# Kernel optimization log

Hardware: AMD Instinct MI355X
Metric: run time of the kernel (lower is better)

The kernel has to match this reference:

```python
import jax, jax.numpy as jnp
import numpy as np

B, N, D = 8, 2048, 512


def setup_inputs() -> dict:
    key = jax.random.key(0)
    ks = jax.random.split(key, 16)
    s = 1.0 / np.sqrt(D)  # ~ torch Linear default init scale
    inp = {
        "X": jax.random.normal(ks[0], (B, N, D), jnp.float32),
        "Y": jax.random.normal(ks[1], (B, N, D), jnp.float32),
    }
    names = ["xq", "xk", "xv", "yq", "yk", "yv"]
    for i, nm in enumerate(names):
        inp[f"W_{nm}"] = jax.random.uniform(ks[2 + 2 * i], (D, D), jnp.float32, -s, s)
        inp[f"b_{nm}"] = jax.random.uniform(ks[3 + 2 * i], (D,), jnp.float32, -s, s)
    return inp


def _lin(x, W, b):
    # torch nn.Linear: x @ W^T + b
    return jnp.einsum("bnd,ed->bne", x, W) + b


def reference(X, Y, W_xq, b_xq, W_xk, b_xk, W_xv, b_xv, W_yq, b_yq, W_yk, b_yk, W_yv, b_yv):
    d = X.shape[-1]
    scale = 1.0 / jnp.sqrt(jnp.asarray(d, X.dtype))
    Q1, K1, V1 = _lin(X, W_xq, b_xq), _lin(X, W_xk, b_xk), _lin(X, W_xv, b_xv)
    Q2, K2, V2 = _lin(Y, W_yq, b_yq), _lin(Y, W_yk, b_yk), _lin(Y, W_yv, b_yv)
    # NOTE: F.softmax called without dim on a 3-D tensor -> torch legacy dim=0 (batch axis).
    S1 = jnp.einsum("bnd,bmd->bnm", Q1, K2) * scale  # [B, N, N]
    A1 = jax.nn.softmax(S1, axis=0)
    U_A1 = X + jnp.einsum("bnm,bmd->bnd", A1, V2)  # dropout = identity (eval)
    S2 = jnp.einsum("bnd,bmd->bnm", Q2, K1) * scale
    A2 = jax.nn.softmax(S2, axis=0)
    U_A2 = Y + jnp.einsum("bnm,bmd->bnd", A2, V1)
    return U_A1 + U_A2
```

## Files before the change

### kernel.cpp

```cpp
#include <hip/hip_runtime.h>

typedef unsigned short u16;
typedef unsigned char u8;
typedef __attribute__((ext_vector_type(8))) short bf16x8;
typedef __attribute__((ext_vector_type(4))) float f32x4;
typedef __attribute__((ext_vector_type(8))) u16 u16x8;
typedef __attribute__((ext_vector_type(2))) int i32x2;
typedef __attribute__((ext_vector_type(2))) float f32x2;

#define GLOAD_LDS(g, s) __builtin_amdgcn_global_load_lds( \
    (const __attribute__((address_space(1))) void*)(g),   \
    (__attribute__((address_space(3))) void*)(s), 16, 0, 0)

__device__ __forceinline__ u16 f2bf(float f) {
  union { float f; unsigned u; } v; v.f = f;
  unsigned r = v.u + 0x7fffu + ((v.u >> 16) & 1u);
  return (u16)(r >> 16);
}
__device__ __forceinline__ float bf2f(u16 h) {
  union { unsigned u; float f; } v; v.u = ((unsigned)h) << 16;
  return v.f;
}

__device__ __forceinline__ unsigned lds_addr(const void* p) {
  return (unsigned)(unsigned long long)(__attribute__((address_space(3))) const void*)p;
}
__device__ __forceinline__ bf16x8 ds128(const void* p) {
  bf16x8 r;
  asm volatile("ds_read_b128 %0, %1" : "=v"(r) : "v"(lds_addr(p)));
  return r;
}
__device__ __forceinline__ i32x2 ds64(const void* p) {
  i32x2 r;
  asm volatile("ds_read_b64 %0, %1" : "=v"(r) : "v"(lds_addr(p)));
  return r;
}
__device__ __forceinline__ bf16x8 cvt8(i32x2 v) {
  f32x2 f0 = __builtin_amdgcn_cvt_pk_f32_fp8(v[0], false);
  f32x2 f1 = __builtin_amdgcn_cvt_pk_f32_fp8(v[0], true);
  f32x2 f2 = __builtin_amdgcn_cvt_pk_f32_fp8(v[1], false);
  f32x2 f3 = __builtin_amdgcn_cvt_pk_f32_fp8(v[1], true);
  unsigned w0, w1, w2, w3;
  asm("v_cvt_pk_bf16_f32 %0, %1, %2" : "=v"(w0) : "v"(f0[0]), "v"(f0[1]));
  asm("v_cvt_pk_bf16_f32 %0, %1, %2" : "=v"(w1) : "v"(f1[0]), "v"(f1[1]));
  asm("v_cvt_pk_bf16_f32 %0, %1, %2" : "=v"(w2) : "v"(f2[0]), "v"(f2[1]));
  asm("v_cvt_pk_bf16_f32 %0, %1, %2" : "=v"(w3) : "v"(f3[0]), "v"(f3[1]));
  union { unsigned w[4]; bf16x8 v8; } u;
  u.w[0] = w0; u.w[1] = w1; u.w[2] = w2; u.w[3] = w3;
  return u.v8;
}

__device__ __forceinline__ void stage_one(const u16* g, int ld, u16* d, int tid) {
  int rw = tid >> 3;
  int gs = ((tid & 7) ^ (rw & 7)) << 3;
  int wb = (tid >> 6) << 9;
#pragma unroll
  for (int p = 0; p < 4; p++)
    GLOAD_LDS(g + (long)(p * 64 + rw) * ld + gs, d + p * 4096 + wb);
}

__device__ __forceinline__ void gemm256d(f32x4 (&acc)[8][4],
    const u16* Ag, int lda, const u16* Bg, int ldb, int nk,
    u16* As, u16* Bs, int tid) {
  const int lane = tid & 63, wid = tid >> 6;
  const int wr = (wid >> 2) << 7;
  const int wc = (wid & 3) << 6;
  const int rl = lane & 15, kg = lane >> 4;
  const int swz0 = (kg ^ (rl & 7)) << 3;
  const int rbA = (wr + rl) * 64, rbB = (wc + rl) * 64;

  stage_one(Ag, lda, As, tid);
  stage_one(Bg, ldb, Bs, tid);
  if (nk > 1) stage_one(Ag + 64, lda, As + 16384, tid);

  int ba = 0;
  for (int t = 0; t < nk; ++t) {
    if (t + 1 < nk) asm volatile("s_waitcnt vmcnt(4)" ::: "memory");
    else            asm volatile("s_waitcnt vmcnt(0)" ::: "memory");
    __builtin_amdgcn_s_barrier();
    if (t + 1 < nk)
      stage_one(Bg + (t + 1) * 64, ldb, Bs + ((t + 1) & 1) * 16384, tid);
    if (t + 2 < nk) {
      int nb = ba + 2; if (nb >= 3) nb -= 3;
      stage_one(Ag + (long)(t + 2) * 64, lda, As + nb * 16384, tid);
    }
    const u16* ab = As + ba * 16384 + rbA;
    const u16* bb = Bs + (t & 1) * 16384 + rbB;
#pragma unroll
    for (int kk = 0; kk < 2; kk++) {
      const int sw = swz0 ^ (kk << 5);
      bf16x8 a[8], b[4];
#pragma unroll
      for (int i = 0; i < 8; i++) a[i] = ds128(ab + i * 1024 + sw);
#pragma unroll
      for (int j = 0; j < 4; j++) b[j] = ds128(bb + j * 1024 + sw);
      asm volatile("s_waitcnt lgkmcnt(0)" ::: "memory");
      __builtin_amdgcn_sched_barrier(0);
      __builtin_amdgcn_s_setprio(1);
#pragma unroll
      for (int i = 0; i < 8; i++)
#pragma unroll
        for (int j = 0; j < 4; j++)
          acc[i][j] = __builtin_amdgcn_mfma_f32_16x16x32_bf16(a[i], b[j], acc[i][j], 0, 0, 0);
      __builtin_amdgcn_s_setprio(0);
      __builtin_amdgcn_sched_barrier(0);
    }
    ba = ba + 1; if (ba == 3) ba = 0;
  }
}

__device__ __forceinline__ void stage_A64(const u8* gA, u8* Ad, int tid) {
#pragma unroll
  for (int pass = 0; pass < 2; pass++) {
    int gid = pass * 512 + tid;
    int row = gid >> 2, g = gid & 3;
    GLOAD_LDS(gA + (long)row * 2048 + ((g ^ (row & 3)) << 4), Ad + (gid << 4));
  }
}
__device__ __forceinline__ void stage_B64(const u16* gB, u8* Bd, int tid) {
#pragma unroll
  for (int pass = 0; pass < 2; pass++) {
    int gid = pass * 512 + tid;
    int row = gid >> 3, g = gid & 7;
    GLOAD_LDS(gB + (long)row * 2048 + ((g ^ (row & 7)) << 3), Bd + (gid << 4));
  }
}

__device__ __forceinline__ void gemm_pv8(f32x4 (&acc)[4][4],
    const u8* Ag, const u16* Bg, u8* As, u8* Bs, int tid) {
  const int lane = tid & 63, wid = tid >> 6;
  const int mq = wid >> 1, nh = wid & 1;
  const int rl = lane & 15, kg = lane >> 4;
  const int nk = 16;
  const int abase = (mq * 64 + rl) * 64 + ((kg & 1) << 3);
  const int bbase = (nh * 64 + rl) * 128;

  stage_A64(Ag, As, tid);
  stage_B64(Bg, Bs, tid);
  stage_A64(Ag + 64, As + 16384, tid);
  int ba = 0;
  for (int t = 0; t < nk; ++t) {
    if (t + 1 < nk) asm volatile("s_waitcnt vmcnt(2)" ::: "memory");
    else            asm volatile("s_waitcnt vmcnt(0)" ::: "memory");
    __builtin_amdgcn_s_barrier();
    if (t + 1 < nk) stage_B64(Bg + (t + 1) * 64, Bs + ((t + 1) & 1) * 16384, tid);
    if (t + 2 < nk) {
      int nb = ba + 2; if (nb >= 3) nb -= 3;
      stage_A64(Ag + (long)(t + 2) * 64, As + nb * 16384, tid);
    }
    const u8* ab = As + ba * 16384 + abase;
    const u8* bb = Bs + (t & 1) * 16384 + bbase;
#pragma unroll
    for (int kk = 0; kk < 2; kk++) {
      const int sa = (((kk << 1) + (kg >> 1)) ^ (rl & 3)) << 4;
      const int sb = (((kk << 2) + kg) ^ (rl & 7)) << 4;
      i32x2 ar[4]; bf16x8 bfr[4];
#pragma unroll
      for (int i = 0; i < 4; i++) ar[i] = ds64(ab + i * 1024 + sa);
#pragma unroll
      for (int j = 0; j < 4; j++) bfr[j] = ds128(bb + j * 2048 + sb);
      asm volatile("s_waitcnt lgkmcnt(0)" ::: "memory");
      __builtin_amdgcn_sched_barrier(0);
      bf16x8 a[4];
#pragma unroll
      for (int i = 0; i < 4; i++) a[i] = cvt8(ar[i]);
      __builtin_amdgcn_s_setprio(1);
#pragma unroll
      for (int i = 0; i < 4; i++)
#pragma unroll
        for (int j = 0; j < 4; j++)
          acc[i][j] = __builtin_amdgcn_mfma_f32_16x16x32_bf16(a[i], bfr[j], acc[i][j], 0, 0, 0);
      __builtin_amdgcn_s_setprio(0);
      __builtin_amdgcn_sched_barrier(0);
    }
    ba = ba + 1; if (ba == 3) ba = 0;
  }
}

__global__ __launch_bounds__(256) void k_cvt2(const float* __restrict__ inX,
                                              const float* __restrict__ inY,
                                              u16* __restrict__ oX, u16* __restrict__ oY,
                                              int n8) {
  int i = blockIdx.x * 256 + threadIdx.x;
  const float* in = (i < n8) ? inX : inY;
  u16* out = (i < n8) ? oX : oY;
  int k = (i < n8) ? i : i - n8;
  const float4* pf = (const float4*)in + (long)k * 2;
  float4 a = pf[0], b = pf[1];
  u16x8 o;
  o[0] = f2bf(a.x); o[1] = f2bf(a.y); o[2] = f2bf(a.z); o[3] = f2bf(a.w);
  o[4] = f2bf(b.x); o[5] = f2bf(b.y); o[6] = f2bf(b.z); o[7] = f2bf(b.w);
  *((u16x8*)out + k) = o;
}

struct P6 { const float* p[6]; };
struct O6 { u16* p[6]; };

__global__ __launch_bounds__(256) void k_cvt_w(P6 w, u16* __restrict__ out) {
  int z = blockIdx.y;
  int i = blockIdx.x * 256 + threadIdx.x;
  const float4* pf = (const float4*)w.p[z] + (long)i * 2;
  float4 a = pf[0], b = pf[1];
  u16x8 o;
  o[0] = f2bf(a.x); o[1] = f2bf(a.y); o[2] = f2bf(a.z); o[3] = f2bf(a.w);
  o[4] = f2bf(b.x); o[5] = f2bf(b.y); o[6] = f2bf(b.z); o[7] = f2bf(b.w);
  *((u16x8*)(out + (long)z * 262144) + i) = o;
}

__global__ __launch_bounds__(512) void k_proj2(const u16* __restrict__ Xb, const u16* __restrict__ Yb,
                                               const u16* __restrict__ Wb, P6 bias, O6 dst) {
  __shared__ u16 As[49152], Bs[32768];
  int x = blockIdx.x;
  int swz = (x & 7) * 96 + (x >> 3);
  int grp = swz >= 384;
  int r = grp ? swz - 384 : swz;
  int bm = r / 6, bn = r - bm * 6;
  int tid = threadIdx.x;
  const u16* Ag = (grp ? Yb : Xb) + (long)bm * 256 * 512;
  const u16* Bg = Wb + (long)grp * 786432 + (long)bn * 256 * 512;
  f32x4 acc[8][4] = {};
  gemm256d(acc, Ag, 512, Bg, 512, 8, As, Bs, tid);
  int z = grp * 3 + (bn >> 1);
  const float* bi = bias.p[z];
  u16* D = dst.p[z];
  int lane = tid & 63, wid = tid >> 6;
  int row0 = bm * 256 + ((wid >> 2) << 7) + ((lane >> 4) << 2);
  int colz = (bn & 1) * 256 + ((wid & 3) << 6) + (lane & 15);
  float bj[4];
#pragma unroll
  for (int j = 0; j < 4; j++) bj[j] = bi[colz + (j << 4)];
#pragma unroll
  for (int i = 0; i < 8; i++)
#pragma unroll
    for (int j = 0; j < 4; j++)
#pragma unroll
      for (int rr = 0; rr < 4; rr++)
        D[(long)(row0 + (i << 4) + rr) * 512 + colz + (j << 4)] = f2bf(acc[i][j][rr] + bj[j]);
}

__global__ __launch_bounds__(512) void k_s(const u16* __restrict__ Q, const u16* __restrict__ K,
                                           u16* __restrict__ S) {
  __shared__ u16 As[49152], Bs[32768];
  int x = blockIdx.x;
  int swz = (x & 7) * 64 + (x >> 3);
  int bn = swz & 7, bm = (swz >> 3) & 7, b = swz >> 6;
  int tid = threadIdx.x;
  const u16* Ag = Q + (long)b * 1048576 + (long)bm * 256 * 512;
  const u16* Bg = K + (long)b * 1048576 + (long)bn * 256 * 512;
  f32x4 acc[8][4] = {};
  gemm256d(acc, Ag, 512, Bg, 512, 8, As, Bs, tid);
  u16* D = S + (long)b * 4194304;
  const float scale = 0.04419417382415922f;
  int lane = tid & 63, wid = tid >> 6;
  int row0 = bm * 256 + ((wid >> 2) << 7) + ((lane >> 4) << 2);
  int col0 = bn * 256 + ((wid & 3) << 6) + (lane & 15);
#pragma unroll
  for (int i = 0; i < 8; i++)
#pragma unroll
    for (int j = 0; j < 4; j++)
#pragma unroll
      for (int rr = 0; rr < 4; rr++)
        D[(long)(row0 + (i << 4) + rr) * 2048 + col0 + (j << 4)] = f2bf(acc[i][j][rr] * scale);
}

__global__ __launch_bounds__(256) void k_softmax8(const u16* __restrict__ S,
                                                  u8* __restrict__ A8) {
  int idx = blockIdx.x * 256 + threadIdx.x;
  u16x8 v[8];
#pragma unroll
  for (int b = 0; b < 8; b++) v[b] = *((const u16x8*)(S + (long)b * 4194304) + idx);
  unsigned w0[8], w1[8];
#pragma unroll
  for (int jp = 0; jp < 4; jp++) {
    float va[8], vb[8];
    {
      float e[8], m = -1e30f;
#pragma unroll
      for (int b = 0; b < 8; b++) { e[b] = bf2f(v[b][2 * jp]); m = fmaxf(m, e[b]); }
      float s = 0.f;
#pragma unroll
      for (int b = 0; b < 8; b++) { e[b] = __expf(e[b] - m); s += e[b]; }
      float inv = 1.0f / s;
#pragma unroll
      for (int b = 0; b < 8; b++) va[b] = e[b] * inv;
    }
    {
      float e[8], m = -1e30f;
#pragma unroll
      for (int b = 0; b < 8; b++) { e[b] = bf2f(v[b][2 * jp + 1]); m = fmaxf(m, e[b]); }
      float s = 0.f;
#pragma unroll
      for (int b = 0; b < 8; b++) { e[b] = __expf(e[b] - m); s += e[b]; }
      float inv = 1.0f / s;
#pragma unroll
      for (int b = 0; b < 8; b++) vb[b] = e[b] * inv;
    }
#pragma unroll
    for (int b = 0; b < 8; b++) {
      if (jp == 0)      w0[b] = __builtin_amdgcn_cvt_pk_fp8_f32(va[b], vb[b], 0,     false);
      else if (jp == 1) w0[b] = __builtin_amdgcn_cvt_pk_fp8_f32(va[b], vb[b], w0[b], true);
      else if (jp == 2) w1[b] = __builtin_amdgcn_cvt_pk_fp8_f32(va[b], vb[b], 0,     false);
      else              w1[b] = __builtin_amdgcn_cvt_pk_fp8_f32(va[b], vb[b], w1[b], true);
    }
  }
#pragma unroll
  for (int b = 0; b < 8; b++) {
    i32x2 w; w[0] = (int)w0[b]; w[1] = (int)w1[b];
    *(i32x2*)(A8 + (long)b * 4194304 + (long)idx * 8) = w;
  }
}

__global__ __launch_bounds__(256) void k_tr(const u16* __restrict__ V1, const u16* __restrict__ V2,
                                            u16* __restrict__ T1, u16* __restrict__ T2) {
  __shared__ u16 tile[64][65];
  int z = blockIdx.z;
  const u16* src = (z < 8 ? V1 : V2) + (long)(z & 7) * 1048576;
  u16*       dst = (z < 8 ? T1 : T2) + (long)(z & 7) * 1048576;
  int n0 = blockIdx.x * 64, d0 = blockIdx.y * 64;
  int t = threadIdx.x;
  int r = t >> 2, cs = (t & 3) * 16;
  const u16x8* sp = (const u16x8*)(src + (long)(n0 + r) * 512 + d0 + cs);
  u16x8 a = sp[0], b = sp[1];
#pragma unroll
  for (int jj = 0; jj < 8; jj++) { tile[r][cs + jj] = a[jj]; tile[r][cs + 8 + jj] = b[jj]; }
  __syncthreads();
  u16x8 o0, o1;
#pragma unroll
  for (int jj = 0; jj < 8; jj++) { o0[jj] = tile[cs + jj][r]; o1[jj] = tile[cs + 8 + jj][r]; }
  u16x8* op = (u16x8*)(dst + (long)(d0 + r) * 2048 + n0 + cs);
  op[0] = o0; op[1] = o1;
}

__global__ __launch_bounds__(512) void k_pv8m(const u8* __restrict__ A2, const u16* __restrict__ Vt1,
                                              const u8* __restrict__ A1, const u16* __restrict__ Vt2,
                                              const float* __restrict__ X, const float* __restrict__ Y,
                                              float* __restrict__ out, float* __restrict__ P) {
  __shared__ u8 As[49152], Bs[32768];
  int x = blockIdx.x;
  int swz = (x & 7) * 64 + (x >> 3);
  int b = swz >> 6;
  int r = swz & 63;
  int bn = r & 3, kc = (r >> 2) & 1, bm = r >> 3;
  int tid = threadIdx.x;
  long aoff = (long)b * 4194304 + (long)bm * 256 * 2048 + kc * 1024;
  long voff = (long)b * 1048576 + (long)bn * 128 * 2048 + kc * 1024;
  f32x4 acc[4][4] = {};
  gemm_pv8(acc, A2 + aoff, Vt1 + voff, As, Bs, tid);
  __builtin_amdgcn_s_barrier();
  gemm_pv8(acc, A1 + aoff, Vt2 + voff, As, Bs, tid);
  int lane = tid & 63, wid = tid >> 6;
  int mq = wid >> 1, nh = wid & 1;
  int row0 = bm * 256 + mq * 64 + ((lane >> 4) << 2);
  int col0 = bn * 128 + nh * 64 + (lane & 15);
  long base = (long)b * 1048576;
#pragma unroll
  for (int i = 0; i < 4; i++)
#pragma unroll
    for (int j = 0; j < 4; j++)
#pragma unroll
      for (int rr = 0; rr < 4; rr++) {
        long idx = base + (long)(row0 + (i << 4) + rr) * 512 + col0 + (j << 4);
        float v = acc[i][j][rr];
        if (kc) P[idx] = v;
        else    out[idx] = v + X[idx] + Y[idx];
      }
}

__global__ __launch_bounds__(256) void k_fin(float* __restrict__ out, const float* __restrict__ P) {
  long i = (long)(blockIdx.x * 256 + threadIdx.x) * 4;
  float4 o = *(const float4*)(out + i);
  float4 p = *(const float4*)(P + i);
  o.x += p.x; o.y += p.y; o.z += p.z; o.w += p.w;
  *(float4*)(out + i) = o;
}

extern "C" void kernel_launch(void* const* d_in, const int* in_sizes, int n_in,
                              void* d_out, int out_size, void* d_ws, size_t ws_size,
                              hipStream_t stream) {
  const float* X = (const float*)d_in[0];
  const float* Y = (const float*)d_in[1];
  P6 wp, bp;
  for (int i = 0; i < 6; i++) { wp.p[i] = (const float*)d_in[2 + 2 * i]; bp.p[i] = (const float*)d_in[3 + 2 * i]; }

  const long NX = 8L * 2048 * 512;
  const long NS = 8L * 2048 * 2048;
  u16* p = (u16*)d_ws;
  u16* Xb = p;  p += NX;
  u16* Yb = p;  p += NX;
  u16* Wb = p;  p += 6L * 512 * 512;
  u16* Q1 = p;  p += NX;
  u16* K2 = p;  p += NX;
  u16* Q2 = p;  p += NX;
  u16* K1 = p;  p += NX;
  u16* Sb = p;  p += NS;
  u16* V1 = Sb;
  u16* V2 = Sb + NX;
  u16* Vt1 = Xb;
  u16* Vt2 = Yb;
  u8* A8_2 = (u8*)Q2;
  u8* A8_1 = (u8*)Q1;
  float* Pbuf = (float*)Sb;
  (void)ws_size; (void)in_sizes; (void)n_in; (void)out_size;

  dim3 T(256);
  k_cvt2<<<dim3(8192), T, 0, stream>>>(X, Y, Xb, Yb, (int)(NX / 8));
  k_cvt_w<<<dim3(128, 6), T, 0, stream>>>(wp, Wb);
  O6 dst; dst.p[0] = Q1; dst.p[1] = K1; dst.p[2] = V1; dst.p[3] = Q2; dst.p[4] = K2; dst.p[5] = V2;
  k_proj2<<<dim3(768), dim3(512), 0, stream>>>(Xb, Yb, Wb, bp, dst);
  k_tr<<<dim3(32, 8, 16), T, 0, stream>>>(V1, V2, Vt1, Vt2);
  k_s<<<dim3(512), dim3(512), 0, stream>>>(Q2, K1, Sb);
  k_softmax8<<<dim3(2048), T, 0, stream>>>(Sb, A8_2);
  k_s<<<dim3(512), dim3(512), 0, stream>>>(Q1, K2, Sb);
  k_softmax8<<<dim3(2048), T, 0, stream>>>(Sb, A8_1);
  k_pv8m<<<dim3(512), dim3(512), 0, stream>>>(A8_2, Vt1, A8_1, Vt2, X, Y, (float*)d_out, Pbuf);
  k_fin<<<dim3((int)(NX / 1024)), T, 0, stream>>>((float*)d_out, Pbuf);
}
```

Baseline: 335.6 us.

## Permute FP8 attention layout so PV GEMM reads A with one 128-bit LDS load

The softmax kernel now writes FP8 attention weights in a permuted column order, so each lane's two k-halves sit next to each other. The PV GEMM can then fetch A with a single ds_read_b128 per row instead of two ds_read_b64, using an adjusted XOR swizzle on both staging and reading. The k-loop is restructured to issue all LDS reads up front and wait only partially (lgkmcnt(4)) before the first MFMA half, overlapping the second B reads with compute. This couples the producer layout to the consumer, and holding more fragments live raises register pressure.

```diff
diff --git a/kernel.cpp b/kernel.cpp
--- a/kernel.cpp
+++ b/kernel.cpp
@@ -6,6 +6,7 @@
 typedef __attribute__((ext_vector_type(4))) float f32x4;
 typedef __attribute__((ext_vector_type(8))) u16 u16x8;
 typedef __attribute__((ext_vector_type(2))) int i32x2;
+typedef __attribute__((ext_vector_type(4))) int i32x4;
 typedef __attribute__((ext_vector_type(2))) float f32x2;
 
 #define GLOAD_LDS(g, s) __builtin_amdgcn_global_load_lds( \
@@ -30,9 +31,9 @@
   asm volatile("ds_read_b128 %0, %1" : "=v"(r) : "v"(lds_addr(p)));
   return r;
 }
-__device__ __forceinline__ i32x2 ds64(const void* p) {
-  i32x2 r;
-  asm volatile("ds_read_b64 %0, %1" : "=v"(r) : "v"(lds_addr(p)));
+__device__ __forceinline__ i32x4 ds128i(const void* p) {
+  i32x4 r;
+  asm volatile("ds_read_b128 %0, %1" : "=v"(r) : "v"(lds_addr(p)));
   return r;
 }
 __device__ __forceinline__ bf16x8 cvt8(i32x2 v) {
@@ -114,7 +115,7 @@
   for (int pass = 0; pass < 2; pass++) {
     int gid = pass * 512 + tid;
     int row = gid >> 2, g = gid & 3;
-    GLOAD_LDS(gA + (long)row * 2048 + ((g ^ (row & 3)) << 4), Ad + (gid << 4));
+    GLOAD_LDS(gA + (long)row * 2048 + ((g ^ ((row >> 1) & 3)) << 4), Ad + (gid << 4));
   }
 }
 __device__ __forceinline__ void stage_B64(const u16* gB, u8* Bd, int tid) {
@@ -132,7 +133,8 @@
   const int mq = wid >> 1, nh = wid & 1;
   const int rl = lane & 15, kg = lane >> 4;
   const int nk = 16;
-  const int abase = (mq * 64 + rl) * 64 + ((kg & 1) << 3);
+  const int abase = (mq * 64 + rl) * 64;
+  const int aswz = (kg ^ ((rl >> 1) & 3)) << 4;
   const int bbase = (nh * 64 + rl) * 128;
 
   stage_A64(Ag, As, tid);
@@ -150,26 +152,39 @@
     }
     const u8* ab = As + ba * 16384 + abase;
     const u8* bb = Bs + (t & 1) * 16384 + bbase;
-#pragma unroll
-    for (int kk = 0; kk < 2; kk++) {
-      const int sa = (((kk << 1) + (kg >> 1)) ^ (rl & 3)) << 4;
-      const int sb = (((kk << 2) + kg) ^ (rl & 7)) << 4;
-      i32x2 ar[4]; bf16x8 bfr[4];
-#pragma unroll
-      for (int i = 0; i < 4; i++) ar[i] = ds64(ab + i * 1024 + sa);
-#pragma unroll
-      for (int j = 0; j < 4; j++) bfr[j] = ds128(bb + j * 2048 + sb);
-      asm volatile("s_waitcnt lgkmcnt(0)" ::: "memory");
-      __builtin_amdgcn_sched_barrier(0);
+    i32x4 a4[4]; bf16x8 b0[4], b1[4];
+#pragma unroll
+    for (int i = 0; i < 4; i++) a4[i] = ds128i(ab + i * 1024 + aswz);
+#pragma unroll
+    for (int j = 0; j < 4; j++) b0[j] = ds128(bb + j * 2048 + ((kg ^ (rl & 7)) << 4));
+#pragma unroll
+    for (int j = 0; j < 4; j++) b1[j] = ds128(bb + j * 2048 + (((4 + kg) ^ (rl & 7)) << 4));
+    asm volatile("s_waitcnt lgkmcnt(4)" ::: "memory");
+    __builtin_amdgcn_sched_barrier(0);
+    {
       bf16x8 a[4];
 #pragma unroll
-      for (int i = 0; i < 4; i++) a[i] = cvt8(ar[i]);
+      for (int i = 0; i < 4; i++) { i32x2 lo; lo[0] = a4[i][0]; lo[1] = a4[i][1]; a[i] = cvt8(lo); }
       __builtin_amdgcn_s_setprio(1);
 #pragma unroll
       for (int i = 0; i < 4; i++)
 #pragma unroll
         for (int j = 0; j < 4; j++)
-          acc[i][j] = __builtin_amdgcn_mfma_f32_16x16x32_bf16(a[i], bfr[j], acc[i][j], 0, 0, 0);
+          acc[i][j] = __builtin_amdgcn_mfma_f32_16x16x32_bf16(a[i], b0[j], acc[i][j], 0, 0, 0);
+      __builtin_amdgcn_s_setprio(0);
+    }
+    asm volatile("s_waitcnt lgkmcnt(0)" ::: "memory");
+    __builtin_amdgcn_sched_barrier(0);
+    {
+      bf16x8 a[4];
+#pragma unroll
+      for (int i = 0; i < 4; i++) { i32x2 hi; hi[0] = a4[i][2]; hi[1] = a4[i][3]; a[i] = cvt8(hi); }
+      __builtin_amdgcn_s_setprio(1);
+#pragma unroll
+      for (int i = 0; i < 4; i++)
+#pragma unroll
+        for (int j = 0; j < 4; j++)
+          acc[i][j] = __builtin_amdgcn_mfma_f32_16x16x32_bf16(a[i], b1[j], acc[i][j], 0, 0, 0);
       __builtin_amdgcn_s_setprio(0);
       __builtin_amdgcn_sched_barrier(0);
     }
@@ -303,10 +318,11 @@
       else              w1[b] = __builtin_amdgcn_cvt_pk_fp8_f32(va[b], vb[b], w1[b], true);
     }
   }
+  long cp = ((long)idx & ~7L) | (((long)idx & 3) << 1) | (((long)idx >> 2) & 1);
 #pragma unroll
   for (int b = 0; b < 8; b++) {
     i32x2 w; w[0] = (int)w0[b]; w[1] = (int)w1[b];
-    *(i32x2*)(A8 + (long)b * 4194304 + (long)idx * 8) = w;
+    *(i32x2*)(A8 + (long)b * 4194304 + cp * 8) = w;
   }
 }
 
```

New measurement: 335.6 us. Within noise of the previous version (-0.0%).
